# Kernel tuning notes

Hardware: AMD Instinct MI355X
Metric: run time of the kernel (lower is better)

The kernel has to match this reference:

```python
import jax, jax.numpy as jnp
import numpy as np

N_NODES = 100000
DEG = 16
N_EDGES = N_NODES * DEG  # 1,600,000
D_IN = 128
D_OUT = 128


def setup_inputs() -> dict:
    key = jax.random.key(0)
    k_x, k_w, k_idx = jax.random.split(key, 3)
    x = jax.random.normal(k_x, (N_NODES, D_IN), dtype=jnp.float32)
    # glorot-uniform linear weight, stored as [in, out] for x @ W
    limit = float(np.sqrt(6.0 / (D_IN + D_OUT)))
    W = jax.random.uniform(k_w, (D_IN, D_OUT), dtype=jnp.float32, minval=-limit, maxval=limit)
    bias = jnp.zeros((D_OUT,), dtype=jnp.float32)
    # valid CSR: fixed out-degree DEG per destination node
    ptr = jnp.arange(N_NODES + 1, dtype=jnp.int64) * DEG
    idx = jax.random.randint(k_idx, (N_EDGES,), 0, N_NODES, dtype=jnp.int64)
    return {"x": x, "W": W, "bias": bias, "ptr": ptr, "idx": idx, "num_node": N_NODES}


def reference(x, W, bias, ptr, idx, num_node):
    # dense projection (lin, no bias inside)
    h = x @ W  # [N, D_OUT]
    E = idx.shape[0]
    deg = ptr[1:] - ptr[:-1]  # [N]
    # destination node id per edge (CSR row expansion)
    dst = jnp.repeat(jnp.arange(num_node, dtype=idx.dtype), deg, total_repeat_length=E)
    # gcn_norm: edge_value[e] = 1/deg(dst[e]), inf -> 0
    inv_deg = jnp.where(deg == 0, 0.0, 1.0 / deg.astype(h.dtype))  # [N]
    edge_value = inv_deg[dst]  # [E]
    # gather-multiply-scatter: out[i] = sum_e ev[e] * h[idx[e]] for e in row i
    gathered = h[idx] * edge_value[:, None]  # [E, D_OUT]
    out = jax.ops.segment_sum(gathered, dst, num_segments=num_node)  # [N, D_OUT]
    return out + bias
```

## Files before the change

kernel.cpp:

```cpp
#include <hip/hip_runtime.h>
#include <hip/hip_bf16.h>


#define NN 100000
#define D 128

using short8 = __attribute__((ext_vector_type(8))) short;
using short4v = __attribute__((ext_vector_type(4))) short;
using f32x4 = __attribute__((ext_vector_type(4))) float;

__device__ __forceinline__ float bf2f(short s) {
  unsigned int u = ((unsigned int)(unsigned short)s) << 16;
  return __builtin_bit_cast(float, u);
}
__device__ __forceinline__ short f2bs(float f) {
  __hip_bfloat16 b = __float2bfloat16(f);
  return *reinterpret_cast<short*>(&b);
}

__global__ __launch_bounds__(256) void gemm_xw(const float* __restrict__ x,
                                               const float* __restrict__ W,
                                               __hip_bfloat16* __restrict__ h) {
  __shared__ __hip_bfloat16 Wl[D][D + 8];
  int tid = threadIdx.x;
  for (int i = tid; i < D * D; i += 256) {
    int k = i >> 7, c = i & 127;
    Wl[c][k] = __float2bfloat16(W[i]);
  }
  __syncthreads();

  int wid = tid >> 6, lane = tid & 63;
  int c16 = lane & 15;
  int kc = lane >> 4;

  const int ntiles = NN / 16;
  for (int t = blockIdx.x * 4 + wid; t < ntiles; t += gridDim.x * 4) {
    int r0 = t * 16;
    const float* xrow = x + (size_t)(r0 + c16) * D + kc * 8;
    short8 a[4];
#pragma unroll
    for (int kk = 0; kk < 4; ++kk) {
      float4 f0 = *reinterpret_cast<const float4*>(xrow + kk * 32);
      float4 f1 = *reinterpret_cast<const float4*>(xrow + kk * 32 + 4);
      a[kk][0] = f2bs(f0.x); a[kk][1] = f2bs(f0.y);
      a[kk][2] = f2bs(f0.z); a[kk][3] = f2bs(f0.w);
      a[kk][4] = f2bs(f1.x); a[kk][5] = f2bs(f1.y);
      a[kk][6] = f2bs(f1.z); a[kk][7] = f2bs(f1.w);
    }

    f32x4 acc[8];
#pragma unroll
    for (int ct = 0; ct < 8; ++ct) acc[ct] = (f32x4)(0.0f);

#pragma unroll
    for (int kk = 0; kk < 4; ++kk) {
#pragma unroll
      for (int ct = 0; ct < 8; ++ct) {
        short8 b = *reinterpret_cast<const short8*>(&Wl[ct * 16 + c16][kk * 32 + kc * 8]);
        acc[ct] = __builtin_amdgcn_mfma_f32_16x16x32_bf16(a[kk], b, acc[ct], 0, 0, 0);
      }
    }

    int rbase = r0 + kc * 4;
#pragma unroll
    for (int ct = 0; ct < 8; ++ct) {
      int col = ct * 16 + c16;
#pragma unroll
      for (int j = 0; j < 4; ++j) {
        h[(size_t)(rbase + j) * D + col] = __float2bfloat16(acc[ct][j]);
      }
    }
  }
}

__global__ __launch_bounds__(256) void agg_2n(const __hip_bfloat16* __restrict__ h,
                                              const int* __restrict__ ptr,
                                              const int* __restrict__ idx,
                                              const float* __restrict__ bias,
                                              float* __restrict__ out) {
  int wv = threadIdx.x >> 6;
  int lane = threadIdx.x & 63;
  int nbase = blockIdx.x * 8 + wv * 2;
  if (nbase >= NN) return;
  int j = lane >> 5;
  int half = (lane >> 4) & 1;
  int sub = lane & 15;
  int node = nbase + j;

  int pv = (lane <= 2) ? ptr[nbase + lane] : 0;
  bool fast = __all(lane > 2 || pv == 16 * (nbase + lane));

  if (fast) {
    int iv = __builtin_nontemporal_load(idx + (size_t)nbase * 16 + (lane & 31));
    int rid[8];
#pragma unroll
    for (int t = 0; t < 8; ++t) rid[t] = __shfl(iv, j * 16 + half + 2 * t);
    short8 v[8];
#pragma unroll
    for (int t = 0; t < 8; ++t)
      v[t] = *reinterpret_cast<const short8*>(h + (size_t)rid[t] * D + sub * 8);

    float acc[8];
#pragma unroll
    for (int q = 0; q < 8; ++q) acc[q] = 0.f;
#pragma unroll
    for (int t = 0; t < 8; ++t)
#pragma unroll
      for (int q = 0; q < 8; ++q) acc[q] += bf2f(v[t][q]);

#pragma unroll
    for (int q = 0; q < 8; ++q) acc[q] += __shfl_xor(acc[q], 16);

    if (half == 0) {
      const float inv = 1.0f / 16.0f;
      const float* bp = bias + sub * 8;
      float4 b0 = *reinterpret_cast<const float4*>(bp);
      float4 b1 = *reinterpret_cast<const float4*>(bp + 4);
      f32x4 r0, r1;
      r0[0] = fmaf(acc[0], inv, b0.x);
      r0[1] = fmaf(acc[1], inv, b0.y);
      r0[2] = fmaf(acc[2], inv, b0.z);
      r0[3] = fmaf(acc[3], inv, b0.w);
      r1[0] = fmaf(acc[4], inv, b1.x);
      r1[1] = fmaf(acc[5], inv, b1.y);
      r1[2] = fmaf(acc[6], inv, b1.z);
      r1[3] = fmaf(acc[7], inv, b1.w);
      f32x4* op = (f32x4*)(out + (size_t)node * D + sub * 8);
      __builtin_nontemporal_store(r0, op);
      __builtin_nontemporal_store(r1, op + 1);
    }
  } else {
    int s32 = lane & 31;
    int p0 = ptr[node], p1 = ptr[node + 1];
    float a0 = 0.f, a1 = 0.f, a2 = 0.f, a3 = 0.f;
    for (int e = p0; e < p1; ++e) {
      int rid = idx[e];
      short4v vv = *reinterpret_cast<const short4v*>(h + (size_t)rid * D + s32 * 4);
      a0 += bf2f(vv[0]);
      a1 += bf2f(vv[1]);
      a2 += bf2f(vv[2]);
      a3 += bf2f(vv[3]);
    }
    int deg = p1 - p0;
    float inv = deg > 0 ? 1.0f / (float)deg : 0.f;
    const float* bp = bias + s32 * 4;
    f32x4 r;
    r[0] = fmaf(a0, inv, bp[0]);
    r[1] = fmaf(a1, inv, bp[1]);
    r[2] = fmaf(a2, inv, bp[2]);
    r[3] = fmaf(a3, inv, bp[3]);
    *(f32x4*)(out + (size_t)node * D + s32 * 4) = r;
  }
}

__global__ __launch_bounds__(256) void agg_x(const float* __restrict__ x,
                                             const int* __restrict__ ptr,
                                             const int* __restrict__ idx,
                                             float* __restrict__ out) {
  int node = blockIdx.x * 4 + (threadIdx.x >> 6);
  int lane = threadIdx.x & 63;
  if (node >= NN) return;
  int p0 = ptr[node], p1 = ptr[node + 1];
  float sx = 0.f, sy = 0.f;
  for (int e = p0; e < p1; ++e) {
    int nid = idx[e];
    const float2 v = ((const float2*)(x + (size_t)nid * D))[lane];
    sx += v.x;
    sy += v.y;
  }
  int deg = p1 - p0;
  float inv = (deg > 0) ? (1.0f / (float)deg) : 0.0f;
  float2 r;
  r.x = sx * inv;
  r.y = sy * inv;
  ((float2*)(out + (size_t)node * D))[lane] = r;
}

__global__ __launch_bounds__(256) void rowgemm_inplace(float* __restrict__ io,
                                                       const float* __restrict__ W,
                                                       const float* __restrict__ bias) {
  __shared__ float4 Wl[D * 32];
  __shared__ float xr[8][D];
  int tid = threadIdx.x;
  for (int i = tid; i < D * 32; i += 256) Wl[i] = ((const float4*)W)[i];
  int r = tid >> 5;
  int c4 = tid & 31;
  float4 b4 = ((const float4*)bias)[c4];
  __syncthreads();
  const int ngroups = NN / 8;
  for (int g = blockIdx.x; g < ngroups; g += gridDim.x) {
    size_t base = (size_t)g * 8;
    ((float4*)xr)[tid] = ((const float4*)(io + base * D))[tid];
    __syncthreads();
    float4 acc = b4;
#pragma unroll 8
    for (int k = 0; k < D; ++k) {
      float xv = xr[r][k];
      float4 w = Wl[k * 32 + c4];
      acc.x = fmaf(xv, w.x, acc.x);
      acc.y = fmaf(xv, w.y, acc.y);
      acc.z = fmaf(xv, w.z, acc.z);
      acc.w = fmaf(xv, w.w, acc.w);
    }
    ((float4*)(io + (base + (size_t)r) * D))[c4] = acc;
    __syncthreads();
  }
}

extern "C" void kernel_launch(void* const* d_in, const int* in_sizes, int n_in,
                              void* d_out, int out_size, void* d_ws, size_t ws_size,
                              hipStream_t stream) {
  const float* x = (const float*)d_in[0];
  const float* W = (const float*)d_in[1];
  const float* bias = (const float*)d_in[2];
  const int* ptr = (const int*)d_in[3];
  const int* idx = (const int*)d_in[4];
  float* out = (float*)d_out;

  const size_t need = (size_t)NN * D * sizeof(__hip_bfloat16);
  if (ws_size >= need) {
    __hip_bfloat16* h = (__hip_bfloat16*)d_ws;
    gemm_xw<<<782, 256, 0, stream>>>(x, W, h);
    agg_2n<<<NN / 8, 256, 0, stream>>>(h, ptr, idx, bias, out);
  } else {
    agg_x<<<NN / 4, 256, 0, stream>>>(x, ptr, idx, out);
    rowgemm_inplace<<<1280, 256, 0, stream>>>(out, W, bias);
  }
}
```

Before: 84.68 us.

## Split projected features into two column-half slabs and aggregate per slab

The GEMM now writes h as two separate 64-column bf16 slabs (each NN x 64), and aggregation blocks alternate between slabs so each block processes 16 nodes over half the feature columns. Each gathered row is 128 bytes instead of 256, which shrinks the working set per slab and is meant to improve L2/MALL hit rates for random neighbour gathers. The cost is more shuffle reductions (three xor stages across 4 nodes per wave), twice as many idx loads overall, and a narrower scalar fallback path.

```diff
diff --git a/kernel.cpp b/kernel.cpp
--- a/kernel.cpp
+++ b/kernel.cpp
@@ -6,7 +6,6 @@
 #define D 128
 
 using short8 = __attribute__((ext_vector_type(8))) short;
-using short4v = __attribute__((ext_vector_type(4))) short;
 using f32x4 = __attribute__((ext_vector_type(4))) float;
 
 __device__ __forceinline__ float bf2f(short s) {
@@ -18,9 +17,9 @@
   return *reinterpret_cast<short*>(&b);
 }
 
-__global__ __launch_bounds__(256) void gemm_xw(const float* __restrict__ x,
-                                               const float* __restrict__ W,
-                                               __hip_bfloat16* __restrict__ h) {
+__global__ __launch_bounds__(256) void gemm_xw_ns2(const float* __restrict__ x,
+                                                   const float* __restrict__ W,
+                                                   __hip_bfloat16* __restrict__ h) {
   __shared__ __hip_bfloat16 Wl[D][D + 8];
   int tid = threadIdx.x;
   for (int i = tid; i < D * D; i += 256) {
@@ -64,92 +63,100 @@
     int rbase = r0 + kc * 4;
 #pragma unroll
     for (int ct = 0; ct < 8; ++ct) {
-      int col = ct * 16 + c16;
+      size_t sb = (size_t)(ct >> 2) * NN;
+      int cc = (ct & 3) * 16 + c16;
 #pragma unroll
       for (int j = 0; j < 4; ++j) {
-        h[(size_t)(rbase + j) * D + col] = __float2bfloat16(acc[ct][j]);
-      }
-    }
-  }
-}
-
-__global__ __launch_bounds__(256) void agg_2n(const __hip_bfloat16* __restrict__ h,
-                                              const int* __restrict__ ptr,
-                                              const int* __restrict__ idx,
-                                              const float* __restrict__ bias,
-                                              float* __restrict__ out) {
+        h[(sb + (rbase + j)) * 64 + cc] = __float2bfloat16(acc[ct][j]);
+      }
+    }
+  }
+}
+
+__global__ __launch_bounds__(256) void agg_ns2(const __hip_bfloat16* __restrict__ h,
+                                               const int* __restrict__ ptr,
+                                               const int* __restrict__ idx,
+                                               const float* __restrict__ bias,
+                                               float* __restrict__ out) {
+  int s = blockIdx.x & 1;
+  int g = blockIdx.x >> 1;
   int wv = threadIdx.x >> 6;
   int lane = threadIdx.x & 63;
-  int nbase = blockIdx.x * 8 + wv * 2;
-  if (nbase >= NN) return;
-  int j = lane >> 5;
-  int half = (lane >> 4) & 1;
-  int sub = lane & 15;
-  int node = nbase + j;
-
-  int pv = (lane <= 2) ? ptr[nbase + lane] : 0;
-  bool fast = __all(lane > 2 || pv == 16 * (nbase + lane));
+  int n0 = g * 16 + wv * 4;
+  if (n0 >= NN) return;
+  int j = lane >> 3;
+  int sub = lane & 7;
+  const size_t sbase = (size_t)s * NN;
+
+  int pv = (lane <= 4) ? ptr[n0 + lane] : 0;
+  bool fast = __all(lane > 4 || pv == 16 * (n0 + lane));
 
   if (fast) {
-    int iv = __builtin_nontemporal_load(idx + (size_t)nbase * 16 + (lane & 31));
+    int iv = __builtin_nontemporal_load(idx + (size_t)n0 * 16 + lane);
     int rid[8];
 #pragma unroll
-    for (int t = 0; t < 8; ++t) rid[t] = __shfl(iv, j * 16 + half + 2 * t);
+    for (int t = 0; t < 8; ++t) rid[t] = __shfl(iv, t * 8 + j);
     short8 v[8];
 #pragma unroll
     for (int t = 0; t < 8; ++t)
-      v[t] = *reinterpret_cast<const short8*>(h + (size_t)rid[t] * D + sub * 8);
-
-    float acc[8];
-#pragma unroll
-    for (int q = 0; q < 8; ++q) acc[q] = 0.f;
-#pragma unroll
-    for (int t = 0; t < 8; ++t)
-#pragma unroll
-      for (int q = 0; q < 8; ++q) acc[q] += bf2f(v[t][q]);
-
-#pragma unroll
-    for (int q = 0; q < 8; ++q) acc[q] += __shfl_xor(acc[q], 16);
-
-    if (half == 0) {
-      const float inv = 1.0f / 16.0f;
-      const float* bp = bias + sub * 8;
-      float4 b0 = *reinterpret_cast<const float4*>(bp);
-      float4 b1 = *reinterpret_cast<const float4*>(bp + 4);
-      f32x4 r0, r1;
-      r0[0] = fmaf(acc[0], inv, b0.x);
-      r0[1] = fmaf(acc[1], inv, b0.y);
-      r0[2] = fmaf(acc[2], inv, b0.z);
-      r0[3] = fmaf(acc[3], inv, b0.w);
-      r1[0] = fmaf(acc[4], inv, b1.x);
-      r1[1] = fmaf(acc[5], inv, b1.y);
-      r1[2] = fmaf(acc[6], inv, b1.z);
-      r1[3] = fmaf(acc[7], inv, b1.w);
-      f32x4* op = (f32x4*)(out + (size_t)node * D + sub * 8);
-      __builtin_nontemporal_store(r0, op);
-      __builtin_nontemporal_store(r1, op + 1);
+      v[t] = *reinterpret_cast<const short8*>(h + (sbase + rid[t]) * 64 + sub * 8);
+
+    float acc[4][8];
+#pragma unroll
+    for (int nl = 0; nl < 4; ++nl)
+#pragma unroll
+      for (int q = 0; q < 8; ++q) acc[nl][q] = 0.f;
+
+#pragma unroll
+    for (int t = 0; t < 8; ++t) {
+#pragma unroll
+      for (int q = 0; q < 8; ++q) acc[t >> 1][q] += bf2f(v[t][q]);
+    }
+
+#pragma unroll
+    for (int nl = 0; nl < 4; ++nl)
+#pragma unroll
+      for (int q = 0; q < 8; ++q) {
+        acc[nl][q] += __shfl_xor(acc[nl][q], 8);
+        acc[nl][q] += __shfl_xor(acc[nl][q], 16);
+        acc[nl][q] += __shfl_xor(acc[nl][q], 32);
+      }
+
+    const float inv = 1.0f / 16.0f;
+    const float* bp = bias + s * 64 + sub * 8;
+    float4 b0 = *reinterpret_cast<const float4*>(bp);
+    float4 b1 = *reinterpret_cast<const float4*>(bp + 4);
+#pragma unroll
+    for (int nl = 0; nl < 4; ++nl) {
+      if (j == nl) {
+        f32x4 r0, r1;
+        r0[0] = fmaf(acc[nl][0], inv, b0.x);
+        r0[1] = fmaf(acc[nl][1], inv, b0.y);
+        r0[2] = fmaf(acc[nl][2], inv, b0.z);
+        r0[3] = fmaf(acc[nl][3], inv, b0.w);
+        r1[0] = fmaf(acc[nl][4], inv, b1.x);
+        r1[1] = fmaf(acc[nl][5], inv, b1.y);
+        r1[2] = fmaf(acc[nl][6], inv, b1.z);
+        r1[3] = fmaf(acc[nl][7], inv, b1.w);
+        f32x4* op = (f32x4*)(out + (size_t)(n0 + nl) * D + s * 64 + sub * 8);
+        __builtin_nontemporal_store(r0, op);
+        __builtin_nontemporal_store(r1, op + 1);
+      }
     }
   } else {
-    int s32 = lane & 31;
-    int p0 = ptr[node], p1 = ptr[node + 1];
-    float a0 = 0.f, a1 = 0.f, a2 = 0.f, a3 = 0.f;
-    for (int e = p0; e < p1; ++e) {
-      int rid = idx[e];
-      short4v vv = *reinterpret_cast<const short4v*>(h + (size_t)rid * D + s32 * 4);
-      a0 += bf2f(vv[0]);
-      a1 += bf2f(vv[1]);
-      a2 += bf2f(vv[2]);
-      a3 += bf2f(vv[3]);
-    }
-    int deg = p1 - p0;
-    float inv = deg > 0 ? 1.0f / (float)deg : 0.f;
-    const float* bp = bias + s32 * 4;
-    f32x4 r;
-    r[0] = fmaf(a0, inv, bp[0]);
-    r[1] = fmaf(a1, inv, bp[1]);
-    r[2] = fmaf(a2, inv, bp[2]);
-    r[3] = fmaf(a3, inv, bp[3]);
-    *(f32x4*)(out + (size_t)node * D + s32 * 4) = r;
+    for (int nl = 0; nl < 4; ++nl) {
+      int node = n0 + nl;
+      int p0 = ptr[node], p1 = ptr[node + 1];
+      float a = 0.f;
+      for (int e = p0; e < p1; ++e) {
+        int rid = idx[e];
+        a += __bfloat162float(h[(sbase + rid) * 64 + lane]);
+      }
+      int deg = p1 - p0;
+      float invd = deg > 0 ? 1.0f / (float)deg : 0.f;
+      int c = s * 64 + lane;
+      out[(size_t)node * D + c] = fmaf(a, invd, bias[c]);
+    }
   }
 }
 
@@ -220,8 +227,8 @@
   const size_t need = (size_t)NN * D * sizeof(__hip_bfloat16);
   if (ws_size >= need) {
     __hip_bfloat16* h = (__hip_bfloat16*)d_ws;
-    gemm_xw<<<782, 256, 0, stream>>>(x, W, h);
-    agg_2n<<<NN / 8, 256, 0, stream>>>(h, ptr, idx, bias, out);
+    gemm_xw_ns2<<<782, 256, 0, stream>>>(x, W, h);
+    agg_ns2<<<(NN / 16) * 2, 256, 0, stream>>>(h, ptr, idx, bias, out);
   } else {
     agg_x<<<NN / 4, 256, 0, stream>>>(x, ptr, idx, out);
     rowgemm_inplace<<<1280, 256, 0, stream>>>(out, W, bias);
```

Result: no change. 84.74 us (+0.1%).
